# Performance work log

Measured on AMD Instinct MI355X. Metric: run time of the kernel, lower is better.

## Reference

```python
import jax, jax.numpy as jnp
import numpy as np

N, IN, H, C, E = 50000, 128, 2, 64, 800000
HC = H * C  # 128
NEG_SLOPE = 0.2
EPS_GN = 1e-5


def setup_inputs() -> dict:
    key = jax.random.key(0)
    ks = jax.random.split(key, 32)
    r = lambda i, shape: jax.random.normal(ks[i], shape, dtype=jnp.float32) * 0.1
    inp = {
        'x': jax.random.normal(ks[0], (N, IN), dtype=jnp.float32),
        'edge_index': jax.random.randint(ks[1], (2, E), 0, N, dtype=jnp.int64),
        # conv 0: in=128 -> heads*emb=128
        'Wl0': r(2, (IN, HC)), 'bl0': jnp.zeros((HC,), jnp.float32),
        'Wr0': r(3, (IN, HC)), 'br0': jnp.zeros((HC,), jnp.float32),
        'att0': r(4, (H, C)), 'bias0': jnp.zeros((HC,), jnp.float32),
        # conv 1: in=128 -> 128
        'Wl1': r(5, (HC, HC)), 'bl1': jnp.zeros((HC,), jnp.float32),
        'Wr1': r(6, (HC, HC)), 'br1': jnp.zeros((HC,), jnp.float32),
        'att1': r(7, (H, C)), 'bias1': jnp.zeros((HC,), jnp.float32),
        # GraphNorm params (weight, bias, mean_scale)
        'g0': jnp.ones((HC,), jnp.float32), 'be0': jnp.zeros((HC,), jnp.float32), 'ms0': jnp.ones((HC,), jnp.float32),
        'g1': jnp.ones((HC,), jnp.float32), 'be1': jnp.zeros((HC,), jnp.float32), 'ms1': jnp.ones((HC,), jnp.float32),
        # MLP head
        'W1': r(8, (HC, C)), 'b1': jnp.zeros((C,), jnp.float32),
        'W2': r(9, (C, 2)), 'b2': jnp.zeros((2,), jnp.float32),
    }
    return inp


def gatv2_conv(x, src, dst, Wl, bl, Wr, br, att, bias):
    # PyG GATv2Conv: separate source/target transforms, edge attention, segment softmax
    xl = (x @ Wl + bl).reshape(N, H, C)  # source features
    xr = (x @ Wr + br).reshape(N, H, C)  # target features
    m = jax.nn.leaky_relu(xl[src] + xr[dst], NEG_SLOPE)  # [Etot, H, C]
    e = jnp.einsum('ehc,hc->eh', m, att)                  # [Etot, H]
    emax = jax.ops.segment_max(e, dst, num_segments=N)    # stable softmax per dst
    ex = jnp.exp(e - emax[dst])
    denom = jax.ops.segment_sum(ex, dst, num_segments=N)
    alpha = ex / (denom[dst] + 1e-16)
    out = jax.ops.segment_sum(xl[src] * alpha[:, :, None], dst, num_segments=N)
    return out.reshape(N, HC) + bias


def graph_norm(x, gamma, beta, mean_scale):
    # PyG GraphNorm with batch=None (single graph)
    mean = x.mean(axis=0)
    out = x - mean_scale * mean
    var = (out * out).mean(axis=0)
    return gamma * out / jnp.sqrt(var + EPS_GN) + beta


def reference(x, edge_index, Wl0, bl0, Wr0, br0, att0, bias0,
              Wl1, bl1, Wr1, br1, att1, bias1,
              g0, be0, ms0, g1, be1, ms1, W1, b1, W2, b2):
    loop = jnp.arange(N, dtype=edge_index.dtype)
    src = jnp.concatenate([edge_index[0], loop])  # add_self_loops=True
    dst = jnp.concatenate([edge_index[1], loop])
    # layer 0 (conv + GraphNorm + ReLU)
    h = jax.nn.relu(graph_norm(gatv2_conv(x, src, dst, Wl0, bl0, Wr0, br0, att0, bias0), g0, be0, ms0))
    # layer 1
    h = jax.nn.relu(graph_norm(gatv2_conv(h, src, dst, Wl1, bl1, Wr1, br1, att1, bias1), g1, be1, ms1))
    # dropout is identity in eval mode
    h = jax.nn.relu(h @ W1 + b1)
    return h @ W2 + b2
```

## Files before the change

### kernel.cpp

```cpp
#include <hip/hip_runtime.h>
#include <hip/hip_bf16.h>

#define N_NODES 50000
#define NE      800000
#define NETOT   (NE + N_NODES)
#define NEG     0.2f
#define NBUCK   196
#define NSEG    64
#define SEGCAP  128
#define NCTR    (NBUCK * NSEG)

typedef unsigned short u16;
typedef unsigned int   u32;
typedef __attribute__((ext_vector_type(8))) short bf16x8;
typedef __attribute__((ext_vector_type(4))) float f32x4;

__device__ __forceinline__ float b2f(u16 v) {
    union { float f; u32 u; } c; c.u = ((u32)v) << 16; return c.f;
}
__device__ __forceinline__ u16 f2b(float f) {
    union { float f; u32 u; } c; c.f = f;
    u32 r = c.u + 0x7FFF + ((c.u >> 16) & 1);
    return (u16)(r >> 16);
}
__device__ __forceinline__ float ldf(const void* p, int i, int fmt) {
    return fmt ? b2f(((const u16*)p)[i]) : ((const float*)p)[i];
}

__device__ __forceinline__ float red16(float p) {
    union { float f; int i; } a, b;
    a.f = p; b.i = __builtin_amdgcn_update_dpp(0, a.i, 0xB1,  0xF, 0xF, true); p += b.f;
    a.f = p; b.i = __builtin_amdgcn_update_dpp(0, a.i, 0x4E,  0xF, 0xF, true); p += b.f;
    a.f = p; b.i = __builtin_amdgcn_update_dpp(0, a.i, 0x141, 0xF, 0xF, true); p += b.f;
    a.f = p; b.i = __builtin_amdgcn_update_dpp(0, a.i, 0x140, 0xF, 0xF, true); p += b.f;
    return p;
}

__device__ __forceinline__ float lrelu(float v) {
    return fmaf(0.4f, fabsf(v), 0.6f * v);
}

__global__ void init_all(const u32* __restrict__ xw, const u32* __restrict__ w0,
                         const int* __restrict__ ei,
                         int* __restrict__ flag, int* __restrict__ bcnt) {
    int g = blockIdx.x * 256 + threadIdx.x;
    if (g < NCTR) bcnt[g] = 0;
    if (blockIdx.x == 0) {
        int wv = threadIdx.x >> 6, l = threadIdx.x & 63;
        if (wv == 0) {
            u32 v = xw[l * 50000 + 1];
            u32 e = (v >> 7) & 0xFF;
            unsigned long long m = __ballot(e >= 100 && e <= 140);
            if (l == 0) { flag[0] = (__popcll(m) >= 48) ? 1 : 0; flag[1] = 0; }
        } else if (wv == 1) {
            u32 v = w0[l * 128 + 1];
            u32 e = (v >> 7) & 0xFF;
            unsigned long long m = __ballot(e >= 100 && e <= 140);
            if (l == 0) flag[3] = (__popcll(m) >= 48) ? 1 : 0;
        } else if (wv == 2) {
            int v = ei[(l * 25000) | 1];
            unsigned long long nz = __ballot(v != 0);
            if (l == 0) flag[2] = (nz == 0ULL) ? 1 : 0;
        }
    }
}

__global__ void bin_a(const int* __restrict__ ei, const int* __restrict__ flag,
                      int* __restrict__ bcnt, u32* __restrict__ pairs) {
    int e = blockIdx.x * 256 + threadIdx.x;
    if (e >= NE) return;
    int f = flag[2];
    int s, d;
    if (f) { s = ei[2 * e]; d = ei[2 * (NE + e)]; }
    else   { s = ei[e];     d = ei[NE + e]; }
    int idx = (d >> 8) * NSEG + (blockIdx.x & (NSEG - 1));
    int pos = atomicAdd(&bcnt[idx], 1);
    if (pos < SEGCAP)
        pairs[(size_t)idx * SEGCAP + pos] = ((u32)(d & 255) << 16) | (u32)s;
}

__global__ __launch_bounds__(256) void bin_b(const u32* __restrict__ pairs,
        const int* __restrict__ bcnt,
        int* __restrict__ indptr, int* __restrict__ srcs) {
    __shared__ int cnt[256];
    __shared__ int scn[256];
    __shared__ int msh[NSEG];
    __shared__ int baseSh;
    int b = blockIdx.x, tid = threadIdx.x;
    int nb0 = b << 8;
    int nodesHere = min(256, N_NODES - nb0);
    if (tid < NSEG) msh[tid] = min(bcnt[b * NSEG + tid], SEGCAP);
    int pre = 0;
    for (int i = tid; i < b * NSEG; i += 256) pre += min(bcnt[i], SEGCAP);
    scn[tid] = pre; __syncthreads();
    for (int off = 128; off > 0; off >>= 1) {
        if (tid < off) scn[tid] += scn[tid + off];
        __syncthreads();
    }
    if (tid == 0) baseSh = scn[0] + nb0;
    __syncthreads();
    int base = baseSh;
    cnt[tid] = (tid < nodesHere) ? 1 : 0;
    __syncthreads();
    const u32* bp = pairs + (size_t)b * NSEG * SEGCAP;
    for (int t = tid; t < NSEG * SEGCAP; t += 256) {
        int seg = t >> 7, i = t & (SEGCAP - 1);
        if (i < msh[seg]) {
            int dloc = (int)(bp[t] >> 16);
            atomicAdd(&cnt[dloc], 1);
        }
    }
    __syncthreads();
    int v = cnt[tid];
    scn[tid] = v; __syncthreads();
    for (int off = 1; off < 256; off <<= 1) {
        int u = (tid >= off) ? scn[tid - off] : 0;
        __syncthreads();
        scn[tid] += u;
        __syncthreads();
    }
    int myoff = base + scn[tid] - v;
    if (tid < nodesHere) indptr[nb0 + tid] = myoff;
    if (tid == 255 && b == NBUCK - 1) indptr[N_NODES] = base + scn[255];
    __syncthreads();
    cnt[tid] = myoff;
    __syncthreads();
    if (tid < nodesHere) {
        int pos = atomicAdd(&cnt[tid], 1);
        srcs[pos] = nb0 + tid;
    }
    for (int t = tid; t < NSEG * SEGCAP; t += 256) {
        int seg = t >> 7, i = t & (SEGCAP - 1);
        if (i < msh[seg]) {
            u32 p = bp[t];
            int pos = atomicAdd(&cnt[p >> 16], 1);
            srcs[pos] = (int)(p & 0xffff);
        }
    }
}

#define LDP 136
#define NT  128
__global__ __launch_bounds__(256) void gemm_xf(const void* __restrict__ inp,
        const int* __restrict__ fin, const int* __restrict__ fw,
        const void* __restrict__ Wl, const void* __restrict__ bl,
        const void* __restrict__ Wr, const void* __restrict__ br,
        const float* __restrict__ nscale, const float* __restrict__ nshift,
        u16* __restrict__ XL, u16* __restrict__ XR) {
    __shared__ u16 As16[NT * LDP];
    __shared__ u16 Bs16[128 * LDP];
    __shared__ float Sc[128], Sh[128];
    int fi = fin[0], fb = fw[0];
    int by = blockIdx.y;
    const void* W  = by ? Wr : Wl;
    const void* bi = by ? br : bl;
    u16* dst       = by ? XR : XL;
    int n0 = blockIdx.x * NT;
    int tid = threadIdx.x;
    bool donorm = (nscale != nullptr);
    if (donorm) {
        if (tid < 128) { Sc[tid] = nscale[tid]; Sh[tid] = nshift[tid]; }
        __syncthreads();
    }
    if (fi) {
        for (int t = tid; t < NT * 16; t += 256) {
            int node = t >> 4, c8 = (t & 15) << 3;
            int n = n0 + node;
            bf16x8 v = {0,0,0,0,0,0,0,0};
            if (n < N_NODES) v = *(const bf16x8*)((const u16*)inp + (size_t)n * 128 + c8);
            *(bf16x8*)&As16[node * LDP + c8] = v;
        }
    } else {
        for (int t = tid; t < NT * 32; t += 256) {
            int node = t >> 5, c4 = (t & 31) << 2;
            int n = n0 + node;
            float4 v = {0.f, 0.f, 0.f, 0.f};
            if (n < N_NODES) v = *(const float4*)((const float*)inp + (size_t)n * 128 + c4);
            if (donorm) {
                v.x = fmaxf(v.x * Sc[c4]     + Sh[c4],     0.f);
                v.y = fmaxf(v.y * Sc[c4 + 1] + Sh[c4 + 1], 0.f);
                v.z = fmaxf(v.z * Sc[c4 + 2] + Sh[c4 + 2], 0.f);
                v.w = fmaxf(v.w * Sc[c4 + 3] + Sh[c4 + 3], 0.f);
            }
            ushort4 h;
            h.x = f2b(v.x); h.y = f2b(v.y); h.z = f2b(v.z); h.w = f2b(v.w);
            *(ushort4*)&As16[node * LDP + c4] = h;
        }
    }
    if (fb) {
        for (int t = tid; t < 128 * 16; t += 256) {
            int k = t >> 4, j8 = (t & 15) << 3;
            bf16x8 v = *(const bf16x8*)((const u16*)W + k * 128 + j8);
            #pragma unroll
            for (int q = 0; q < 8; ++q) Bs16[(j8 + q) * LDP + k] = (u16)v[q];
        }
    } else {
        for (int t = tid; t < 128 * 32; t += 256) {
            int k = t >> 5, j4 = (t & 31) << 2;
            float4 v = *(const float4*)((const float*)W + k * 128 + j4);
            Bs16[(j4 + 0) * LDP + k] = f2b(v.x);
            Bs16[(j4 + 1) * LDP + k] = f2b(v.y);
            Bs16[(j4 + 2) * LDP + k] = f2b(v.z);
            Bs16[(j4 + 3) * LDP + k] = f2b(v.w);
        }
    }
    __syncthreads();

    int wv = tid >> 6, lane = tid & 63;
    int quad = lane >> 4, r = lane & 15;
    int m0 = wv * 32;
    f32x4 acc[2][8];
    #pragma unroll
    for (int mt = 0; mt < 2; ++mt)
        #pragma unroll
        for (int jt = 0; jt < 8; ++jt) acc[mt][jt] = (f32x4){0.f, 0.f, 0.f, 0.f};
    #pragma unroll
    for (int ks = 0; ks < 4; ++ks) {
        int ko = ks * 32 + quad * 8;
        bf16x8 af0 = *(const bf16x8*)&As16[(m0 + r) * LDP + ko];
        bf16x8 af1 = *(const bf16x8*)&As16[(m0 + 16 + r) * LDP + ko];
        #pragma unroll
        for (int jt = 0; jt < 8; ++jt) {
            bf16x8 bfr = *(const bf16x8*)&Bs16[(jt * 16 + r) * LDP + ko];
            acc[0][jt] = __builtin_amdgcn_mfma_f32_16x16x32_bf16(af0, bfr, acc[0][jt], 0, 0, 0);
            acc[1][jt] = __builtin_amdgcn_mfma_f32_16x16x32_bf16(af1, bfr, acc[1][jt], 0, 0, 0);
        }
    }
    __syncthreads();
    #pragma unroll
    for (int jt = 0; jt < 8; ++jt) {
        int j = jt * 16 + r;
        float bj = ldf(bi, j, fb);
        #pragma unroll
        for (int mt = 0; mt < 2; ++mt) {
            #pragma unroll
            for (int reg = 0; reg < 4; ++reg) {
                As16[(m0 + mt * 16 + quad * 4 + reg) * LDP + j] = f2b(acc[mt][jt][reg] + bj);
            }
        }
    }
    __syncthreads();
    #pragma unroll
    for (int rep = 0; rep < 8; ++rep) {
        int idx = rep * 256 + tid;
        int node = idx >> 4, c8 = (idx & 15) << 3;
        int n = n0 + node;
        if (n < N_NODES) {
            bf16x8 v = *(const bf16x8*)&As16[node * LDP + c8];
            *(bf16x8*)(dst + (size_t)n * 128 + c8) = v;
        }
    }
}

__global__ __launch_bounds__(256) void agg_kernel(const u16* __restrict__ XL,
        const u16* __restrict__ XR, const void* __restrict__ att,
        const int* __restrict__ fmt,
        const int* __restrict__ indptr, const int* __restrict__ srcs,
        float4* __restrict__ OUT4) {
    int lane = threadIdx.x & 63;
    int n = blockIdx.x * 4 + (threadIdx.x >> 6);
    if (n >= N_NODES) return;
    int eh = lane >> 5, q = lane & 31;
    int fb = fmt[0];
    ushort4 xrv = *(const ushort4*)(XR + (size_t)n * 128 + q * 4);
    float xr0 = b2f(xrv.x), xr1 = b2f(xrv.y), xr2 = b2f(xrv.z), xr3 = b2f(xrv.w);
    float a0 = ldf(att, 4 * q,     fb);
    float a1 = ldf(att, 4 * q + 1, fb);
    float a2 = ldf(att, 4 * q + 2, fb);
    float a3 = ldf(att, 4 * q + 3, fb);
    int beg = indptr[n], end = indptr[n + 1];
    float acc0 = 0.f, acc1 = 0.f, acc2 = 0.f, acc3 = 0.f, dsum = 0.f;
    int nit = (end - beg + 5) / 6;
    for (int it = 0; it < nit; ++it) {
        int iA = beg + 6 * it + eh;
        int iB = iA + 2;
        int iC = iA + 4;
        bool vA = (iA < end), vB = (iB < end), vC = (iC < end);
        int sA = vA ? srcs[iA] : 0;
        int sB = vB ? srcs[iB] : 0;
        int sC = vC ? srcs[iC] : 0;
        ushort4 xa = *(const ushort4*)(XL + (size_t)sA * 128 + q * 4);
        ushort4 xb = *(const ushort4*)(XL + (size_t)sB * 128 + q * 4);
        ushort4 xc = *(const ushort4*)(XL + (size_t)sC * 128 + q * 4);
        float A0 = b2f(xa.x), A1 = b2f(xa.y), A2 = b2f(xa.z), A3 = b2f(xa.w);
        float B0 = b2f(xb.x), B1 = b2f(xb.y), B2v = b2f(xb.z), B3 = b2f(xb.w);
        float C0 = b2f(xc.x), C1 = b2f(xc.y), C2 = b2f(xc.z), C3 = b2f(xc.w);
        float tA0 = lrelu(A0 + xr0);
        float tA1 = lrelu(A1 + xr1);
        float tA2 = lrelu(A2 + xr2);
        float tA3 = lrelu(A3 + xr3);
        float tB0 = lrelu(B0 + xr0);
        float tB1 = lrelu(B1 + xr1);
        float tB2 = lrelu(B2v + xr2);
        float tB3 = lrelu(B3 + xr3);
        float tC0 = lrelu(C0 + xr0);
        float tC1 = lrelu(C1 + xr1);
        float tC2 = lrelu(C2 + xr2);
        float tC3 = lrelu(C3 + xr3);
        float pA = tA0 * a0;
        pA = fmaf(tA1, a1, pA); pA = fmaf(tA2, a2, pA); pA = fmaf(tA3, a3, pA);
        float pB = tB0 * a0;
        pB = fmaf(tB1, a1, pB); pB = fmaf(tB2, a2, pB); pB = fmaf(tB3, a3, pB);
        float pC = tC0 * a0;
        pC = fmaf(tC1, a1, pC); pC = fmaf(tC2, a2, pC); pC = fmaf(tC3, a3, pC);
        pA = red16(pA);
        pB = red16(pB);
        pC = red16(pC);
        float wA = vA ? __expf(fminf(pA, 60.f)) : 0.f;
        float wB = vB ? __expf(fminf(pB, 60.f)) : 0.f;
        float wC = vC ? __expf(fminf(pC, 60.f)) : 0.f;
        acc0 = fmaf(wA, A0, acc0); acc1 = fmaf(wA, A1, acc1);
        acc2 = fmaf(wA, A2, acc2); acc3 = fmaf(wA, A3, acc3);
        acc0 = fmaf(wB, B0, acc0); acc1 = fmaf(wB, B1, acc1);
        acc2 = fmaf(wB, B2v, acc2); acc3 = fmaf(wB, B3, acc3);
        acc0 = fmaf(wC, C0, acc0); acc1 = fmaf(wC, C1, acc1);
        acc2 = fmaf(wC, C2, acc2); acc3 = fmaf(wC, C3, acc3);
        dsum += wA + wB + wC;
    }
    acc0 += __shfl_xor(acc0, 32);
    acc1 += __shfl_xor(acc1, 32);
    acc2 += __shfl_xor(acc2, 32);
    acc3 += __shfl_xor(acc3, 32);
    dsum += __shfl_xor(dsum, 32);
    if (eh == 0) {
        float inv = 1.f / (dsum + 1e-16f);
        float4 o; o.x = acc0 * inv; o.y = acc1 * inv; o.z = acc2 * inv; o.w = acc3 * inv;
        OUT4[(size_t)n * 32 + q] = o;
    }
}

__global__ __launch_bounds__(256) void colstats(const float* __restrict__ OUT,
        const void* __restrict__ bias, const int* __restrict__ fmt,
        float* __restrict__ Sp1, float* __restrict__ Sp2) {
    __shared__ float sh1[256], sh2[256];
    int tid = threadIdx.x;
    int c = tid & 127, half = tid >> 7;
    float bf = ldf(bias, c, fmt[0]);
    float s1 = 0.f, s2 = 0.f;
    for (int r = blockIdx.x * 2 + half; r < N_NODES; r += gridDim.x * 2) {
        float t = OUT[r * 128 + c] + bf;
        s1 += t; s2 += t * t;
    }
    sh1[tid] = s1; sh2[tid] = s2; __syncthreads();
    if (tid < 128) {
        Sp1[blockIdx.x * 128 + tid] = sh1[tid] + sh1[tid + 128];
        Sp2[blockIdx.x * 128 + tid] = sh2[tid] + sh2[tid + 128];
    }
}

__global__ __launch_bounds__(256) void finalize_norm(const float* __restrict__ Sp1,
        const float* __restrict__ Sp2,
        const void* __restrict__ gamma, const void* __restrict__ beta,
        const void* __restrict__ msc, const void* __restrict__ bias,
        const int* __restrict__ fmt,
        float* __restrict__ scaleA, float* __restrict__ shiftB) {
    __shared__ float sh1[256], sh2[256];
    int c = blockIdx.x, tid = threadIdx.x;
    sh1[tid] = Sp1[tid * 128 + c];
    sh2[tid] = Sp2[tid * 128 + c];
    __syncthreads();
    for (int off = 128; off > 0; off >>= 1) {
        if (tid < off) { sh1[tid] += sh1[tid + off]; sh2[tid] += sh2[tid + off]; }
        __syncthreads();
    }
    if (tid == 0) {
        int fb = fmt[0];
        const float invN = 1.f / (float)N_NODES;
        float mean = sh1[0] * invN;
        float ex2  = sh2[0] * invN;
        float ms = ldf(msc, c, fb);
        float var = ex2 - 2.f * ms * mean * mean + ms * ms * mean * mean;
        float rstd = rsqrtf(var + 1e-5f);
        float A = ldf(gamma, c, fb) * rstd;
        scaleA[c] = A;
        shiftB[c] = ldf(beta, c, fb) - A * (ms * mean - ldf(bias, c, fb));
    }
}

__global__ __launch_bounds__(256) void mlp_kernel(const float* __restrict__ H,
        const void* __restrict__ w1, const void* __restrict__ b1,
        const void* __restrict__ w2, const void* __restrict__ b2,
        const float* __restrict__ nscale, const float* __restrict__ nshift,
        const int* __restrict__ fmt,
        float* __restrict__ out) {
    __shared__ float W1s[128 * 64];
    __shared__ float W2s[128];
    __shared__ float b1s[64];
    __shared__ float Sc[128], Sh[128];
    int tid = threadIdx.x;
    int fb = fmt[0];
    if (fb) {
        for (int t = tid; t < 128 * 8; t += 256) {
            int row8 = t << 3;
            bf16x8 v = *(const bf16x8*)((const u16*)w1 + row8);
            #pragma unroll
            for (int q = 0; q < 8; ++q) W1s[row8 + q] = b2f((u16)v[q]);
        }
    } else {
        for (int t = tid; t < 128 * 64; t += 256) W1s[t] = ((const float*)w1)[t];
    }
    if (tid < 128) { W2s[tid] = ldf(w2, tid, fb); Sc[tid] = nscale[tid]; Sh[tid] = nshift[tid]; }
    if (tid < 64)  b1s[tid] = ldf(b1, tid, fb);
    __syncthreads();
    int n = blockIdx.x * 256 + tid;
    if (n >= N_NODES) return;
    float z[64];
    #pragma unroll
    for (int j = 0; j < 64; j++) z[j] = b1s[j];
    for (int kb = 0; kb < 128; kb += 16) {
        float h[16];
        #pragma unroll
        for (int t = 0; t < 4; t++) {
            float4 v = *(const float4*)&H[n * 128 + kb + t * 4];
            int c = kb + t * 4;
            h[4 * t]     = fmaxf(v.x * Sc[c]     + Sh[c],     0.f);
            h[4 * t + 1] = fmaxf(v.y * Sc[c + 1] + Sh[c + 1], 0.f);
            h[4 * t + 2] = fmaxf(v.z * Sc[c + 2] + Sh[c + 2], 0.f);
            h[4 * t + 3] = fmaxf(v.w * Sc[c + 3] + Sh[c + 3], 0.f);
        }
        #pragma unroll
        for (int i = 0; i < 16; i++) {
            float hv = h[i];
            const float* wrow = &W1s[(kb + i) * 64];
            #pragma unroll
            for (int j = 0; j < 64; j += 4) {
                const float4 w = *(const float4*)&wrow[j];
                z[j]     += hv * w.x;
                z[j + 1] += hv * w.y;
                z[j + 2] += hv * w.z;
                z[j + 3] += hv * w.w;
            }
        }
    }
    float o0 = ldf(b2, 0, fb), o1 = ldf(b2, 1, fb);
    #pragma unroll
    for (int j = 0; j < 64; j++) {
        float zr = fmaxf(z[j], 0.f);
        o0 += zr * W2s[j * 2];
        o1 += zr * W2s[j * 2 + 1];
    }
    if (o0 != o0) o0 = 12345.f;
    if (o1 != o1) o1 = 12345.f;
    float2 o; o.x = o0; o.y = o1;
    ((float2*)out)[n] = o;
}

extern "C" void kernel_launch(void* const* d_in, const int* in_sizes, int n_in,
                              void* d_out, int out_size, void* d_ws, size_t ws_size,
                              hipStream_t stream) {
    (void)in_sizes; (void)n_in; (void)out_size; (void)ws_size;
    const void* x    = d_in[0];
    const int*  ei   = (const int*)d_in[1];
    const void* Wl0  = d_in[2];
    const void* bl0  = d_in[3];
    const void* Wr0  = d_in[4];
    const void* br0  = d_in[5];
    const void* att0 = d_in[6];
    const void* bias0= d_in[7];
    const void* Wl1  = d_in[8];
    const void* bl1  = d_in[9];
    const void* Wr1  = d_in[10];
    const void* br1  = d_in[11];
    const void* att1 = d_in[12];
    const void* bias1= d_in[13];
    const void* g0   = d_in[14];
    const void* be0  = d_in[15];
    const void* ms0  = d_in[16];
    const void* g1   = d_in[17];
    const void* be1  = d_in[18];
    const void* ms1  = d_in[19];
    const void* W1   = d_in[20];
    const void* b1   = d_in[21];
    const void* W2   = d_in[22];
    const void* b2   = d_in[23];

    char* ws = (char*)d_ws;
    const size_t NF2 = (size_t)N_NODES * 128 * 2;
    const size_t NF4 = (size_t)N_NODES * 128 * 4;
    u16*   XLb = (u16*)(ws);
    u16*   XRb = (u16*)(ws + NF2);
    float* B2  = (float*)(ws + 2 * NF2);
    u32*   pairs = (u32*)B2;
    char* small = ws + 2 * NF2 + NF4;
    float* scaleA = (float*)(small + 1024);
    float* shiftB = (float*)(small + 1536);
    int*   flag   = (int*)(small + 2048);
    float* Sp1    = (float*)(small + 4096);
    float* Sp2    = (float*)(small + 4096 + 131072);
    int*   bcnt   = (int*)(small + 4096 + 262144);
    int*   indptr = (int*)(small + 4096 + 262144 + 50176);
    int*   srcs   = indptr + (N_NODES + 64);

    const int* fX   = &flag[0];
    const int* fFP  = &flag[1];
    const int* fPar = &flag[3];

    init_all<<<(NCTR + 255) / 256, 256, 0, stream>>>((const u32*)x, (const u32*)Wl0,
                                                     ei, flag, bcnt);
    bin_a<<<(NE + 255) / 256, 256, 0, stream>>>(ei, flag, bcnt, pairs);
    bin_b<<<NBUCK, 256, 0, stream>>>(pairs, bcnt, indptr, srcs);

    dim3 ggemm((N_NODES + NT - 1) / NT, 2);

    for (int layer = 0; layer < 2; ++layer) {
        const void* Wl = layer ? Wl1 : Wl0;  const void* bl = layer ? bl1 : bl0;
        const void* Wr = layer ? Wr1 : Wr0;  const void* br = layer ? br1 : br0;
        const void* at = layer ? att1 : att0;
        const void* bi = layer ? bias1 : bias0;
        const void* gm = layer ? g1 : g0;    const void* bt = layer ? be1 : be0;
        const void* mS = layer ? ms1 : ms0;
        const void* inp = layer ? (const void*)B2 : x;
        const int* fin  = layer ? fFP : fX;
        const float* ns = layer ? scaleA : nullptr;
        const float* nh = layer ? shiftB : nullptr;

        gemm_xf<<<ggemm, 256, 0, stream>>>(inp, fin, fPar, Wl, bl, Wr, br, ns, nh,
                                           XLb, XRb);
        agg_kernel<<<(N_NODES + 3) / 4, 256, 0, stream>>>(XLb, XRb, at, fPar, indptr, srcs,
                                               (float4*)B2);
        colstats<<<256, 256, 0, stream>>>(B2, bi, fPar, Sp1, Sp2);
        finalize_norm<<<128, 256, 0, stream>>>(Sp1, Sp2, gm, bt, mS, bi, fPar,
                                               scaleA, shiftB);
    }

    mlp_kernel<<<(N_NODES + 255) / 256, 256, 0, stream>>>(B2, W1, b1, W2, b2,
                                                          scaleA, shiftB, fPar,
                                                          (float*)d_out);
}
```

Baseline: 448.2 us.

## Fuse GraphNorm column statistics into aggregation kernel and widen edge unroll

Removes the separate colstats pass by having each aggregation block reduce its four nodes' biased outputs and squares in shared memory, then atomically add them into 256 slotted partial-sum buffers. The finalize kernel zeroes the slots after reading so layer 1 can reuse them, and init_all zeroes them at the start. The edge loop is also widened from 3 to 6 gathers in flight per half-wave to expose more memory parallelism. This costs atomic contention and extra registers, and drops the early return, which relies on N being divisible by 4.

```diff
diff --git a/kernel.cpp b/kernel.cpp
--- a/kernel.cpp
+++ b/kernel.cpp
@@ -9,6 +9,7 @@
 #define NSEG    64
 #define SEGCAP  128
 #define NCTR    (NBUCK * NSEG)
+#define NSLOT   256
 
 typedef unsigned short u16;
 typedef unsigned int   u32;
@@ -42,9 +43,13 @@
 
 __global__ void init_all(const u32* __restrict__ xw, const u32* __restrict__ w0,
                          const int* __restrict__ ei,
-                         int* __restrict__ flag, int* __restrict__ bcnt) {
+                         int* __restrict__ flag, int* __restrict__ bcnt,
+                         float* __restrict__ Sp1, float* __restrict__ Sp2) {
     int g = blockIdx.x * 256 + threadIdx.x;
     if (g < NCTR) bcnt[g] = 0;
+    for (int i = g; i < NSLOT * 128; i += gridDim.x * 256) {
+        Sp1[i] = 0.f; Sp2[i] = 0.f;
+    }
     if (blockIdx.x == 0) {
         int wv = threadIdx.x >> 6, l = threadIdx.x & 63;
         if (wv == 0) {
@@ -254,12 +259,16 @@
 
 __global__ __launch_bounds__(256) void agg_kernel(const u16* __restrict__ XL,
         const u16* __restrict__ XR, const void* __restrict__ att,
+        const void* __restrict__ bias,
         const int* __restrict__ fmt,
         const int* __restrict__ indptr, const int* __restrict__ srcs,
-        float4* __restrict__ OUT4) {
+        float4* __restrict__ OUT4,
+        float* __restrict__ Sp1, float* __restrict__ Sp2) {
+    __shared__ float shS1[4 * 128];
+    __shared__ float shS2[4 * 128];
     int lane = threadIdx.x & 63;
-    int n = blockIdx.x * 4 + (threadIdx.x >> 6);
-    if (n >= N_NODES) return;
+    int wv = threadIdx.x >> 6;
+    int n = blockIdx.x * 4 + wv;
     int eh = lane >> 5, q = lane & 31;
     int fb = fmt[0];
     ushort4 xrv = *(const ushort4*)(XR + (size_t)n * 128 + q * 4);
@@ -270,52 +279,33 @@
     float a3 = ldf(att, 4 * q + 3, fb);
     int beg = indptr[n], end = indptr[n + 1];
     float acc0 = 0.f, acc1 = 0.f, acc2 = 0.f, acc3 = 0.f, dsum = 0.f;
-    int nit = (end - beg + 5) / 6;
+    int nit = (end - beg + 11) / 12;
     for (int it = 0; it < nit; ++it) {
-        int iA = beg + 6 * it + eh;
-        int iB = iA + 2;
-        int iC = iA + 4;
-        bool vA = (iA < end), vB = (iB < end), vC = (iC < end);
-        int sA = vA ? srcs[iA] : 0;
-        int sB = vB ? srcs[iB] : 0;
-        int sC = vC ? srcs[iC] : 0;
-        ushort4 xa = *(const ushort4*)(XL + (size_t)sA * 128 + q * 4);
-        ushort4 xb = *(const ushort4*)(XL + (size_t)sB * 128 + q * 4);
-        ushort4 xc = *(const ushort4*)(XL + (size_t)sC * 128 + q * 4);
-        float A0 = b2f(xa.x), A1 = b2f(xa.y), A2 = b2f(xa.z), A3 = b2f(xa.w);
-        float B0 = b2f(xb.x), B1 = b2f(xb.y), B2v = b2f(xb.z), B3 = b2f(xb.w);
-        float C0 = b2f(xc.x), C1 = b2f(xc.y), C2 = b2f(xc.z), C3 = b2f(xc.w);
-        float tA0 = lrelu(A0 + xr0);
-        float tA1 = lrelu(A1 + xr1);
-        float tA2 = lrelu(A2 + xr2);
-        float tA3 = lrelu(A3 + xr3);
-        float tB0 = lrelu(B0 + xr0);
-        float tB1 = lrelu(B1 + xr1);
-        float tB2 = lrelu(B2v + xr2);
-        float tB3 = lrelu(B3 + xr3);
-        float tC0 = lrelu(C0 + xr0);
-        float tC1 = lrelu(C1 + xr1);
-        float tC2 = lrelu(C2 + xr2);
-        float tC3 = lrelu(C3 + xr3);
-        float pA = tA0 * a0;
-        pA = fmaf(tA1, a1, pA); pA = fmaf(tA2, a2, pA); pA = fmaf(tA3, a3, pA);
-        float pB = tB0 * a0;
-        pB = fmaf(tB1, a1, pB); pB = fmaf(tB2, a2, pB); pB = fmaf(tB3, a3, pB);
-        float pC = tC0 * a0;
-        pC = fmaf(tC1, a1, pC); pC = fmaf(tC2, a2, pC); pC = fmaf(tC3, a3, pC);
-        pA = red16(pA);
-        pB = red16(pB);
-        pC = red16(pC);
-        float wA = vA ? __expf(fminf(pA, 60.f)) : 0.f;
-        float wB = vB ? __expf(fminf(pB, 60.f)) : 0.f;
-        float wC = vC ? __expf(fminf(pC, 60.f)) : 0.f;
-        acc0 = fmaf(wA, A0, acc0); acc1 = fmaf(wA, A1, acc1);
-        acc2 = fmaf(wA, A2, acc2); acc3 = fmaf(wA, A3, acc3);
-        acc0 = fmaf(wB, B0, acc0); acc1 = fmaf(wB, B1, acc1);
-        acc2 = fmaf(wB, B2v, acc2); acc3 = fmaf(wB, B3, acc3);
-        acc0 = fmaf(wC, C0, acc0); acc1 = fmaf(wC, C1, acc1);
-        acc2 = fmaf(wC, C2, acc2); acc3 = fmaf(wC, C3, acc3);
-        dsum += wA + wB + wC;
+        int ib = beg + 12 * it + eh;
+        bool val[6]; int sv[6]; ushort4 xv[6];
+        #pragma unroll
+        for (int u = 0; u < 6; ++u) {
+            int i = ib + 2 * u;
+            val[u] = (i < end);
+            sv[u] = val[u] ? srcs[i] : 0;
+        }
+        #pragma unroll
+        for (int u = 0; u < 6; ++u)
+            xv[u] = *(const ushort4*)(XL + (size_t)sv[u] * 128 + q * 4);
+        #pragma unroll
+        for (int u = 0; u < 6; ++u) {
+            float X0 = b2f(xv[u].x), X1 = b2f(xv[u].y);
+            float X2 = b2f(xv[u].z), X3 = b2f(xv[u].w);
+            float p = lrelu(X0 + xr0) * a0;
+            p = fmaf(lrelu(X1 + xr1), a1, p);
+            p = fmaf(lrelu(X2 + xr2), a2, p);
+            p = fmaf(lrelu(X3 + xr3), a3, p);
+            p = red16(p);
+            float w = val[u] ? __expf(fminf(p, 60.f)) : 0.f;
+            acc0 = fmaf(w, X0, acc0); acc1 = fmaf(w, X1, acc1);
+            acc2 = fmaf(w, X2, acc2); acc3 = fmaf(w, X3, acc3);
+            dsum += w;
+        }
     }
     acc0 += __shfl_xor(acc0, 32);
     acc1 += __shfl_xor(acc1, 32);
@@ -326,30 +316,28 @@
         float inv = 1.f / (dsum + 1e-16f);
         float4 o; o.x = acc0 * inv; o.y = acc1 * inv; o.z = acc2 * inv; o.w = acc3 * inv;
         OUT4[(size_t)n * 32 + q] = o;
-    }
-}
-
-__global__ __launch_bounds__(256) void colstats(const float* __restrict__ OUT,
-        const void* __restrict__ bias, const int* __restrict__ fmt,
-        float* __restrict__ Sp1, float* __restrict__ Sp2) {
-    __shared__ float sh1[256], sh2[256];
+        float t0 = o.x + ldf(bias, 4 * q,     fb);
+        float t1 = o.y + ldf(bias, 4 * q + 1, fb);
+        float t2 = o.z + ldf(bias, 4 * q + 2, fb);
+        float t3 = o.w + ldf(bias, 4 * q + 3, fb);
+        float4 s1; s1.x = t0; s1.y = t1; s1.z = t2; s1.w = t3;
+        float4 s2; s2.x = t0 * t0; s2.y = t1 * t1; s2.z = t2 * t2; s2.w = t3 * t3;
+        *(float4*)&shS1[wv * 128 + q * 4] = s1;
+        *(float4*)&shS2[wv * 128 + q * 4] = s2;
+    }
+    __syncthreads();
     int tid = threadIdx.x;
-    int c = tid & 127, half = tid >> 7;
-    float bf = ldf(bias, c, fmt[0]);
-    float s1 = 0.f, s2 = 0.f;
-    for (int r = blockIdx.x * 2 + half; r < N_NODES; r += gridDim.x * 2) {
-        float t = OUT[r * 128 + c] + bf;
-        s1 += t; s2 += t * t;
-    }
-    sh1[tid] = s1; sh2[tid] = s2; __syncthreads();
     if (tid < 128) {
-        Sp1[blockIdx.x * 128 + tid] = sh1[tid] + sh1[tid + 128];
-        Sp2[blockIdx.x * 128 + tid] = sh2[tid] + sh2[tid + 128];
-    }
-}
-
-__global__ __launch_bounds__(256) void finalize_norm(const float* __restrict__ Sp1,
-        const float* __restrict__ Sp2,
+        float s1 = shS1[tid] + shS1[128 + tid] + shS1[256 + tid] + shS1[384 + tid];
+        float s2 = shS2[tid] + shS2[128 + tid] + shS2[256 + tid] + shS2[384 + tid];
+        int slot = blockIdx.x & (NSLOT - 1);
+        atomicAdd(&Sp1[slot * 128 + tid], s1);
+        atomicAdd(&Sp2[slot * 128 + tid], s2);
+    }
+}
+
+__global__ __launch_bounds__(256) void finalize_norm(float* __restrict__ Sp1,
+        float* __restrict__ Sp2,
         const void* __restrict__ gamma, const void* __restrict__ beta,
         const void* __restrict__ msc, const void* __restrict__ bias,
         const int* __restrict__ fmt,
@@ -358,6 +346,8 @@
     int c = blockIdx.x, tid = threadIdx.x;
     sh1[tid] = Sp1[tid * 128 + c];
     sh2[tid] = Sp2[tid * 128 + c];
+    Sp1[tid * 128 + c] = 0.f;
+    Sp2[tid * 128 + c] = 0.f;
     __syncthreads();
     for (int off = 128; off > 0; off >>= 1) {
         if (tid < off) { sh1[tid] += sh1[tid + off]; sh2[tid] += sh2[tid + off]; }
@@ -496,7 +486,7 @@
     const int* fPar = &flag[3];
 
     init_all<<<(NCTR + 255) / 256, 256, 0, stream>>>((const u32*)x, (const u32*)Wl0,
-                                                     ei, flag, bcnt);
+                                                     ei, flag, bcnt, Sp1, Sp2);
     bin_a<<<(NE + 255) / 256, 256, 0, stream>>>(ei, flag, bcnt, pairs);
     bin_b<<<NBUCK, 256, 0, stream>>>(pairs, bcnt, indptr, srcs);
 
@@ -516,9 +506,8 @@
 
         gemm_xf<<<ggemm, 256, 0, stream>>>(inp, fin, fPar, Wl, bl, Wr, br, ns, nh,
                                            XLb, XRb);
-        agg_kernel<<<(N_NODES + 3) / 4, 256, 0, stream>>>(XLb, XRb, at, fPar, indptr, srcs,
-                                               (float4*)B2);
-        colstats<<<256, 256, 0, stream>>>(B2, bi, fPar, Sp1, Sp2);
+        agg_kernel<<<(N_NODES + 3) / 4, 256, 0, stream>>>(XLb, XRb, at, bi, fPar,
+                                               indptr, srcs, (float4*)B2, Sp1, Sp2);
         finalize_norm<<<128, 256, 0, stream>>>(Sp1, Sp2, gm, bt, mS, bi, fPar,
                                                scaleA, shiftB);
     }
```

Result: faster. 415.2 us (-7.4%).
